# Performance work log

Measured on AMD Instinct MI355X. Metric: run time of the kernel, lower is better.

The kernel has to match this reference:

```python
import jax, jax.numpy as jnp
import numpy as np

B, T, NS, NC, M = 256, 128, 12, 4, 6
MU = 0.1                 # barrier parameter alg.mu
REG_BASE = 1.6           # fp.reg_exp_base
REG = 2.0                # bp.reg
REG_FAC = REG_BASE ** REG - 1.0


def _mt(a):
    return jnp.swapaxes(a, -1, -2)


def setup_inputs():
    key = jax.random.key(0)
    k = jax.random.split(key, 18)
    rn = lambda i, shape: jax.random.normal(k[i], shape, dtype=jnp.float32)
    eye_s = jnp.eye(NS, dtype=jnp.float32)
    eye_c = jnp.eye(NC, dtype=jnp.float32)
    fx = 0.9 * eye_s + 0.02 * rn(0, (B, T, NS, NS))
    fu = 0.1 * rn(1, (B, T, NS, NC))
    fxx = 0.01 * rn(2, (B, T, NS, NS, NS))
    fxu = 0.01 * rn(3, (B, T, NS, NS, NC))
    fuu = 0.01 * rn(4, (B, T, NS, NC, NC))
    qx = 0.1 * rn(5, (B, T, NS))
    qu = 0.1 * rn(6, (B, T, NC))
    Ax = 0.1 * rn(7, (B, T, NS, NS))
    qxx = eye_s + Ax @ _mt(Ax)            # PSD stage cost Hessian
    Au = 0.1 * rn(8, (B, T, NC, NC))
    quu = eye_c + Au @ _mt(Au)            # PD control Hessian
    qxu = 0.05 * rn(9, (B, T, NS, NC))
    cx = 0.1 * rn(10, (B, T, M, NS))
    cu = 0.1 * rn(11, (B, T, M, NC))
    # feasible iterate: c < 0 strictly, dual s > 0
    c = -(jax.random.uniform(k[12], (B, T, M), dtype=jnp.float32) + 0.1)
    s = 0.05 + 0.1 * jax.random.uniform(k[13], (B, T, M), dtype=jnp.float32)
    px = 0.1 * rn(14, (B, NS))
    P = 0.1 * rn(15, (B, NS, NS))
    pxx = eye_s + P @ _mt(P)              # PSD terminal Hessian
    return {"qx": qx, "qu": qu, "qxx": qxx, "qxu": qxu, "quu": quu,
            "fx": fx, "fu": fu, "fxx": fxx, "fxu": fxu, "fuu": fuu,
            "cx": cx, "cu": cu, "c": c, "s": s, "px": px, "pxx": pxx}


def _backward_pass(qx, qu, qxx, qxu, quu, fx, fu, fxx, fxu, fuu, cx, cu, c, s, px, pxx):
    """Feasible-branch ipddp Riccati backward recursion over T steps, batched over B."""
    Bsz = qx.shape[0]

    def step(carry, inp):
        Vx, Vxx, dV0, dV1, qu_err, mu_err = carry
        (qx_t, qu_t, qxx_t, qxu_t, quu_t, fx_t, fu_t,
         fxx_t, fxu_t, fuu_t, cx_t, cu_t, c_t, s_t) = inp
        s_col = s_t[..., None]                      # (B,M,1)
        c_col = c_t[..., None]                      # (B,M,1)
        # Q-function expansions
        Qx = qx_t[..., None] + _mt(cx_t) @ s_col + _mt(fx_t) @ Vx       # (B,NS,1)
        Qu = qu_t[..., None] + _mt(cu_t) @ s_col + _mt(fu_t) @ Vx       # (B,NC,1)
        fxV = _mt(fx_t) @ Vxx
        v = Vx[..., 0]                              # (B,NS)
        Qxx = qxx_t + fxV @ fx_t + jnp.einsum('bs,bsij->bij', v, fxx_t)
        Qxu = qxu_t + fxV @ fu_t + jnp.einsum('bs,bsij->bij', v, fxu_t)
        Quu = quu_t + _mt(fu_t) @ Vxx @ fu_t + jnp.einsum('bs,bsij->bij', v, fuu_t)
        Quu = 0.5 * (Quu + _mt(Quu))
        Quu_reg = Quu + quu_t * REG_FAC
        # interior-point (feasible) modifications
        r = s_col * c_col + MU                      # (B,M,1)
        cinv = 1.0 / c_col
        sc = (s_t / c_t)[..., None]                 # diag(SCinv) entries
        SCcu = sc * cu_t                            # SCinv @ cu
        SCcx = sc * cx_t                            # SCinv @ cx
        cuSCcu = _mt(cu_t) @ SCcu
        Qu = Qu - _mt(cu_t) @ (cinv * r)
        tempQux = _mt(Qxu) - _mt(cu_t) @ SCcx       # (B,NC,NS)
        rhs = jnp.concatenate([Qu, tempQux], axis=-1)   # (B,NC,1+NS)
        kK = -jnp.linalg.solve(Quu_reg - cuSCcu, rhs)
        ku = kK[..., :1]                            # (B,NC,1)
        Ku = kK[..., 1:]                            # (B,NC,NS)
        cuku = cu_t @ ku                            # (B,M,1)
        ks = (-cinv * (r + s_col * cuku))[..., 0]   # (B,M)
        Ks = -(sc * (cx_t + cu_t @ Ku))             # (B,M,NS)
        Quu2 = Quu - cuSCcu
        Qxu2 = _mt(tempQux)
        Qxx2 = Qxx - _mt(cx_t) @ SCcx
        Qx2 = Qx - _mt(cx_t) @ (cinv * r)
        dV0 = dV0 + (_mt(ku) @ Qu)[..., 0, 0]
        dV1 = dV1 + 0.5 * (_mt(ku) @ Quu2 @ ku)[..., 0, 0]
        QxuKu = Qxu2 @ Ku
        KtQ = _mt(Ku) @ Quu2
        Vx_new = Qx2 + _mt(Ku) @ Qu + KtQ @ ku + Qxu2 @ ku
        Vxx_new = Qxx2 + _mt(QxuKu) + QxuKu + KtQ @ Ku
        Vxx_new = 0.5 * (Vxx_new + _mt(Vxx_new))
        qu_err = jnp.maximum(qu_err, jnp.max(jnp.abs(Qu)))
        mu_err = jnp.maximum(mu_err, jnp.max(jnp.abs(r)))
        return (Vx_new, Vxx_new, dV0, dV1, qu_err, mu_err), (ku[..., 0], Ku, ks, Ks)

    xs = tuple(jnp.moveaxis(a, 1, 0) for a in
               (qx, qu, qxx, qxu, quu, fx, fu, fxx, fxu, fuu, cx, cu, c, s))
    zero = jnp.zeros((), jnp.float32)
    init = (px[..., None], pxx, jnp.zeros((Bsz,), jnp.float32),
            jnp.zeros((Bsz,), jnp.float32), zero, zero)
    carry, outs = jax.lax.scan(step, init, xs, reverse=True)
    Vx, Vxx, dV0, dV1, qu_err, mu_err = carry
    ku, Ku, ks, Ks = (jnp.moveaxis(o, 0, 1) for o in outs)
    dV = jnp.stack([dV0, dV1], axis=-1)             # (B,2)
    opterr = jnp.maximum(qu_err, mu_err)            # c_err == 0 in feasible branch
    return ku, Ku, ks, Ks, dV, opterr, Vx[..., 0], Vxx


def reference(qx, qu, qxx, qxu, quu, fx, fu, fxx, fxu, fuu, cx, cu, c, s, px, pxx):
    return _backward_pass(qx, qu, qxx, qxu, quu, fx, fu, fxx, fxu, fuu,
                          cx, cu, c, s, px, pxx)
```

## Files before the change

### kernel.cpp

```cpp
#include <hip/hip_runtime.h>
#include <cstdint>
#include <cstddef>

#define B_  256
#define T_  128
#define NS_ 12
#define NC_ 4
#define M_  6

constexpr float MU_F      = 0.1f;
constexpr float REG_FAC_F = (float)(1.6 * 1.6 - 1.0);

#define OF_FX   0
#define OF_FU   144
#define OF_FXX  192
#define OF_FXU  1920
#define OF_FUU  2496
#define OF_QXX  2688
#define OF_QXU  2832
#define OF_QUU  2880
#define OF_QX   2896
#define OF_QU   2908
#define OF_CX   2912
#define OF_CU   2984
#define OF_C    3008
#define OF_S    3014
#define STG_N   3020

#define O_KU    0
#define O_KUBIG 131072
#define O_KS    1703936
#define O_KSBIG 1900544
#define O_DV    4259840
#define O_OPT   4260352
#define O_VX    4260353
#define O_VXX   4263425

__device__ __forceinline__ void bar_lds() {
    asm volatile("s_waitcnt lgkmcnt(0)\n\ts_barrier" ::: "memory");
}

__device__ __forceinline__ void gl_lds16(const float* g, float* l) {
    __builtin_amdgcn_global_load_lds((const __attribute__((address_space(1))) void*)g,
                                     (__attribute__((address_space(3))) void*)l, 16, 0, 0);
}
__device__ __forceinline__ void gl_lds4(const float* g, float* l) {
    __builtin_amdgcn_global_load_lds((const __attribute__((address_space(1))) void*)g,
                                     (__attribute__((address_space(3))) void*)l, 4, 0, 0);
}

__global__ __launch_bounds__(256) void ddp_backward(
    const float* __restrict__ qx,  const float* __restrict__ qu,
    const float* __restrict__ qxx, const float* __restrict__ qxu,
    const float* __restrict__ quu, const float* __restrict__ fx,
    const float* __restrict__ fu,  const float* __restrict__ fxx,
    const float* __restrict__ fxu, const float* __restrict__ fuu,
    const float* __restrict__ cx,  const float* __restrict__ cu,
    const float* __restrict__ c_,  const float* __restrict__ s_,
    const float* __restrict__ px,  const float* __restrict__ pxx,
    float* __restrict__ out, float* __restrict__ ws)
{
    const int tid  = threadIdx.x;
    const int b    = blockIdx.x;
    const int lane = tid & 63;
    const int wv   = tid >> 6;

    __shared__ float stg[2][STG_N];
    __shared__ float sVx[12], sVxx[144];
    __shared__ float sfxV[144], sfuV[48];
    __shared__ float sQxx[144], sQxu[48];
    __shared__ float sQuuR[16], sQuu2[16], sM4[16];
    __shared__ float stQux[48];
    __shared__ float sQxb[12], sQub[4], sQu[4], sQx2[12];
    __shared__ float sr[6], scinv[6], ssc[6];
    __shared__ float sKu[48], sku[4], sKtQ[48];
    __shared__ float sAcc[4];

    const float* srcs[14] = {qx, qu, qxx, qxu, quu, fx, fu, fxx, fxu, fuu, cx, cu, c_, s_};

    auto prefetch = [&](float* dst, int tt) {
        const size_t bt = (size_t)b * T_ + tt;
        constexpr int ch_arr[22]  = {5,6,7,7,7,7,7,7,7,8,8,8,9,2,3,4,0,1,10,11,12,13};
        constexpr int ch_goff[22] = {0,0,0,256,512,768,1024,1280,1536,0,256,512,0,0,0,0,0,0,0,0,0,0};
        constexpr int ch_loff[22] = {OF_FX, OF_FU,
                                     OF_FXX, OF_FXX+256, OF_FXX+512, OF_FXX+768,
                                     OF_FXX+1024, OF_FXX+1280, OF_FXX+1536,
                                     OF_FXU, OF_FXU+256, OF_FXU+512,
                                     OF_FUU, OF_QXX, OF_QXU, OF_QUU, OF_QX, OF_QU,
                                     OF_CX, OF_CU, OF_C, OF_S};
        constexpr int ch_nb[22]   = {576,192,1024,1024,1024,1024,1024,1024,768,
                                     1024,1024,256,768,576,192,64,48,16,288,96,24,24};
        constexpr int sl[14]      = {12,4,144,48,16,144,48,1728,576,192,72,24,6,6};
        #pragma unroll
        for (int ci = 0; ci < 22; ++ci) {
            if ((ci & 3) == wv) {
                const float* g = srcs[ch_arr[ci]] + bt * (size_t)sl[ch_arr[ci]] + ch_goff[ci];
                float* l = dst + ch_loff[ci];
                if ((ch_nb[ci] & 15) == 0) {
                    if (lane * 16 < ch_nb[ci]) gl_lds16(g + lane * 4, l);
                } else {
                    if (lane * 4  < ch_nb[ci]) gl_lds4 (g + lane,     l);
                }
            }
        }
    };

    if (tid < 144) sVxx[tid] = pxx[(size_t)b * 144 + tid];
    if (tid < 12)  sVx[tid]  = px[(size_t)b * 12 + tid];
    if (tid == 0)  { sAcc[0] = 0.f; sAcc[1] = 0.f; sAcc[2] = 0.f; sAcc[3] = 0.f; }
    prefetch(stg[0], T_ - 1);
    __syncthreads();

    int cur = 0;
    for (int t = T_ - 1; t >= 0; --t) {
        const float* S = stg[cur];
        if (t > 0) prefetch(stg[cur ^ 1], t - 1);
        const size_t bt = (size_t)b * T_ + t;

        if (tid < 144) {
            const int i = tid / 12, k = tid % 12;
            float acc = 0.f;
            #pragma unroll
            for (int m = 0; m < 12; ++m) acc += S[OF_FX + m*12 + i] * sVxx[m*12 + k];
            sfxV[tid] = acc;
        } else if (tid < 192) {
            const int idx = tid - 144, a = idx / 12, k = idx % 12;
            float acc = 0.f;
            #pragma unroll
            for (int m = 0; m < 12; ++m) acc += S[OF_FU + m*4 + a] * sVxx[m*12 + k];
            sfuV[idx] = acc;
        } else if (tid < 198) {
            const int k = tid - 192;
            const float cc = S[OF_C + k], ssv = S[OF_S + k];
            sr[k] = ssv * cc + MU_F;
            scinv[k] = 1.0f / cc;
            ssc[k] = ssv / cc;
        } else if (tid < 210) {
            const int i = tid - 198;
            float acc = S[OF_QX + i];
            #pragma unroll
            for (int k = 0; k < 6; ++k)  acc += S[OF_CX + k*12 + i] * S[OF_S + k];
            #pragma unroll
            for (int m = 0; m < 12; ++m) acc += S[OF_FX + m*12 + i] * sVx[m];
            sQxb[i] = acc;
        } else if (tid < 214) {
            const int a = tid - 210;
            float acc = S[OF_QU + a];
            #pragma unroll
            for (int k = 0; k < 6; ++k)  acc += S[OF_CU + k*4 + a] * S[OF_S + k];
            #pragma unroll
            for (int m = 0; m < 12; ++m) acc += S[OF_FU + m*4 + a] * sVx[m];
            sQub[a] = acc;
        }
        bar_lds();

        if (tid < 144) {
            const int i = tid / 12, j = tid % 12; (void)j;
            float acc = S[OF_QXX + tid];
            #pragma unroll
            for (int k = 0; k < 12; ++k) acc += sfxV[i*12 + k] * S[OF_FX + k*12 + (tid % 12)];
            #pragma unroll
            for (int ss2 = 0; ss2 < 12; ++ss2) acc += sVx[ss2] * S[OF_FXX + ss2*144 + tid];
            sQxx[tid] = acc;
        } else if (tid < 192) {
            const int idx = tid - 144, i = idx / 4, j = idx % 4;
            float acc = S[OF_QXU + idx];
            #pragma unroll
            for (int k = 0; k < 12; ++k) acc += sfxV[i*12 + k] * S[OF_FU + k*4 + j];
            #pragma unroll
            for (int ss2 = 0; ss2 < 12; ++ss2) acc += sVx[ss2] * S[OF_FXU + ss2*48 + idx];
            sQxu[idx] = acc;
        } else if (tid < 208) {
            const int idx = tid - 192, a = idx / 4, b2 = idx % 4;
            float acc = S[OF_QUU + idx];
            #pragma unroll
            for (int k = 0; k < 12; ++k) acc += sfuV[a*12 + k] * S[OF_FU + k*4 + b2];
            #pragma unroll
            for (int ss2 = 0; ss2 < 12; ++ss2) acc += sVx[ss2] * S[OF_FUU + ss2*16 + idx];
            sQuuR[idx] = acc;
        }
        bar_lds();

        if (tid < 144) {
            const int i = tid / 12, j = tid % 12;
            float acc = sQxx[tid];
            #pragma unroll
            for (int k = 0; k < 6; ++k) acc -= S[OF_CX + k*12 + i] * ssc[k] * S[OF_CX + k*12 + j];
            sQxx[tid] = acc;
        } else if (tid < 192) {
            const int idx = tid - 144, a = idx / 12, i = idx % 12;
            float acc = sQxu[i*4 + a];
            #pragma unroll
            for (int k = 0; k < 6; ++k) acc -= S[OF_CU + k*4 + a] * ssc[k] * S[OF_CX + k*12 + i];
            stQux[idx] = acc;
        } else if (tid < 208) {
            const int idx = tid - 192, a = idx / 4, b2 = idx % 4;
            const float q = 0.5f * (sQuuR[idx] + sQuuR[b2*4 + a]);
            float cs = 0.f;
            #pragma unroll
            for (int k = 0; k < 6; ++k) cs += ssc[k] * S[OF_CU + k*4 + a] * S[OF_CU + k*4 + b2];
            const float q2 = q - cs;
            sQuu2[idx] = q2;
            sM4[idx]   = q2 + S[OF_QUU + idx] * REG_FAC_F;
        } else if (tid < 212) {
            const int a = tid - 208;
            float acc = sQub[a];
            #pragma unroll
            for (int k = 0; k < 6; ++k) acc -= S[OF_CU + k*4 + a] * scinv[k] * sr[k];
            sQu[a] = acc;
        } else if (tid < 224) {
            const int i = tid - 212;
            float acc = sQxb[i];
            #pragma unroll
            for (int k = 0; k < 6; ++k) acc -= S[OF_CX + k*12 + i] * scinv[k] * sr[k];
            sQx2[i] = acc;
        }
        bar_lds();

        if (tid < 13) {
            float a00=sM4[0],  a01=sM4[1],  a02=sM4[2],  a03=sM4[3];
            float a10=sM4[4],  a11=sM4[5],  a12=sM4[6],  a13=sM4[7];
            float a20=sM4[8],  a21=sM4[9],  a22=sM4[10], a23=sM4[11];
            float a30=sM4[12], a31=sM4[13], a32=sM4[14], a33=sM4[15];
            const float i0 = 1.0f / a00;
            const float l10 = a10*i0, l20 = a20*i0, l30 = a30*i0;
            a11 -= l10*a01; a12 -= l10*a02; a13 -= l10*a03;
            a21 -= l20*a01; a22 -= l20*a02; a23 -= l20*a03;
            a31 -= l30*a01; a32 -= l30*a02; a33 -= l30*a03;
            const float i1 = 1.0f / a11;
            const float l21 = a21*i1, l31 = a31*i1;
            a22 -= l21*a12; a23 -= l21*a13;
            a32 -= l31*a12; a33 -= l31*a13;
            const float i2 = 1.0f / a22;
            const float l32 = a32*i2;
            a33 -= l32*a23;

            float r0, r1, r2, r3;
            if (tid == 0) { r0 = sQu[0]; r1 = sQu[1]; r2 = sQu[2]; r3 = sQu[3]; }
            else { const int i = tid - 1; r0 = stQux[i]; r1 = stQux[12+i]; r2 = stQux[24+i]; r3 = stQux[36+i]; }

            const float y0 = r0;
            const float y1 = r1 - l10*y0;
            const float y2 = r2 - l20*y0 - l21*y1;
            const float y3 = r3 - l30*y0 - l31*y1 - l32*y2;
            float x3 = y3 / a33;
            float x2 = (y2 - a23*x3) * i2;
            float x1 = (y1 - a12*x2 - a13*x3) * i1;
            float x0 = (y0 - a01*x1 - a02*x2 - a03*x3) * i0;
            x0 = -x0; x1 = -x1; x2 = -x2; x3 = -x3;

            if (tid == 0) {
                sku[0]=x0; sku[1]=x1; sku[2]=x2; sku[3]=x3;
                float* kg = out + O_KU + bt*4;
                kg[0]=x0; kg[1]=x1; kg[2]=x2; kg[3]=x3;
            } else {
                const int i = tid - 1;
                sKu[i]=x0; sKu[12+i]=x1; sKu[24+i]=x2; sKu[36+i]=x3;
                float* Kg = out + O_KUBIG + bt*48;
                Kg[i]=x0; Kg[12+i]=x1; Kg[24+i]=x2; Kg[36+i]=x3;
            }
        }
        bar_lds();

        if (tid < 48) {
            const int i = tid / 4, a = tid % 4;
            float acc = 0.f;
            #pragma unroll
            for (int b2 = 0; b2 < 4; ++b2) acc += sKu[b2*12 + i] * sQuu2[b2*4 + a];
            sKtQ[tid] = acc;
        } else if (tid < 54) {
            const int k = tid - 48;
            float cuku = 0.f;
            #pragma unroll
            for (int a = 0; a < 4; ++a) cuku += S[OF_CU + k*4 + a] * sku[a];
            out[O_KS + bt*6 + k] = -scinv[k] * (sr[k] + S[OF_S + k] * cuku);
        } else if (tid < 126) {
            const int idx = tid - 54, k = idx / 12, i = idx % 12;
            float acc = S[OF_CX + k*12 + i];
            #pragma unroll
            for (int a = 0; a < 4; ++a) acc += S[OF_CU + k*4 + a] * sKu[a*12 + i];
            out[O_KSBIG + bt*72 + idx] = -(ssc[k] * acc);
        } else if (tid == 126) {
            float d = 0.f;
            #pragma unroll
            for (int a = 0; a < 4; ++a) d += sku[a] * sQu[a];
            sAcc[0] += d;
        } else if (tid == 127) {
            float d = 0.f;
            #pragma unroll
            for (int a = 0; a < 4; ++a)
                #pragma unroll
                for (int b2 = 0; b2 < 4; ++b2) d += sku[a] * sQuu2[a*4 + b2] * sku[b2];
            sAcc[1] += 0.5f * d;
        } else if (tid == 128) {
            float m = 0.f;
            #pragma unroll
            for (int a = 0; a < 4; ++a) m = fmaxf(m, fabsf(sQu[a]));
            sAcc[2] = fmaxf(sAcc[2], m);
        } else if (tid == 129) {
            float m = 0.f;
            #pragma unroll
            for (int k = 0; k < 6; ++k) m = fmaxf(m, fabsf(sr[k]));
            sAcc[3] = fmaxf(sAcc[3], m);
        }
        bar_lds();

        if (tid < 144) {
            const int i = tid / 12, j = tid % 12;
            const float v1 = sQxx[i*12 + j], v2 = sQxx[j*12 + i];
            float qk = 0.f, kk1 = 0.f, kk2 = 0.f;
            #pragma unroll
            for (int a = 0; a < 4; ++a) {
                const float kui = sKu[a*12 + i], kuj = sKu[a*12 + j];
                qk  += stQux[a*12 + i] * kuj + stQux[a*12 + j] * kui;
                kk1 += sKtQ[i*4 + a] * kuj;
                kk2 += sKtQ[j*4 + a] * kui;
            }
            sVxx[tid] = 0.5f * (v1 + v2) + qk + 0.5f * (kk1 + kk2);
        } else if (tid < 156) {
            const int i = tid - 144;
            float acc = sQx2[i];
            #pragma unroll
            for (int a = 0; a < 4; ++a)
                acc += sKu[a*12 + i] * sQu[a] + sKtQ[i*4 + a] * sku[a] + stQux[a*12 + i] * sku[a];
            sVx[i] = acc;
        }
        __syncthreads();
        cur ^= 1;
    }

    if (tid == 0) {
        out[O_DV + b*2 + 0] = sAcc[0];
        out[O_DV + b*2 + 1] = sAcc[1];
        ws[b] = fmaxf(sAcc[2], sAcc[3]);
    }
    if (tid < 12)  out[O_VX + b*12 + tid] = sVx[tid];
    if (tid < 144) out[O_VXX + (size_t)b*144 + tid] = sVxx[tid];
}

__global__ __launch_bounds__(256) void opt_reduce(const float* __restrict__ ws,
                                                  float* __restrict__ out)
{
    float v = ws[threadIdx.x];
    #pragma unroll
    for (int o = 32; o > 0; o >>= 1) v = fmaxf(v, __shfl_down(v, o, 64));
    __shared__ float m[4];
    if ((threadIdx.x & 63) == 0) m[threadIdx.x >> 6] = v;
    __syncthreads();
    if (threadIdx.x == 0) out[O_OPT] = fmaxf(fmaxf(m[0], m[1]), fmaxf(m[2], m[3]));
}

extern "C" void kernel_launch(void* const* d_in, const int* in_sizes, int n_in,
                              void* d_out, int out_size, void* d_ws, size_t ws_size,
                              hipStream_t stream) {
    const float* qx  = (const float*)d_in[0];
    const float* qu  = (const float*)d_in[1];
    const float* qxx = (const float*)d_in[2];
    const float* qxu = (const float*)d_in[3];
    const float* quu = (const float*)d_in[4];
    const float* fx  = (const float*)d_in[5];
    const float* fu  = (const float*)d_in[6];
    const float* fxx = (const float*)d_in[7];
    const float* fxu = (const float*)d_in[8];
    const float* fuu = (const float*)d_in[9];
    const float* cx  = (const float*)d_in[10];
    const float* cu  = (const float*)d_in[11];
    const float* c_  = (const float*)d_in[12];
    const float* s_  = (const float*)d_in[13];
    const float* px  = (const float*)d_in[14];
    const float* pxx = (const float*)d_in[15];
    float* out = (float*)d_out;
    float* ws  = (float*)d_ws;

    hipLaunchKernelGGL(ddp_backward, dim3(B_), dim3(256), 0, stream,
                       qx, qu, qxx, qxu, quu, fx, fu, fxx, fxu, fuu,
                       cx, cu, c_, s_, px, pxx, out, ws);
    hipLaunchKernelGGL(opt_reduce, dim3(1), dim3(256), 0, stream, ws, out);
}
```

Before: 806.0 us.

## Collapse per-batch block to a single wavefront with register-blocked float4 stages

Shrinks each batch block from four wavefronts to one 64-lane wavefront. Because all lanes are in one wave, s_barrier calls become plain lgkmcnt waits. The stages are reorganised so each lane computes four outputs with float4 LDS loads, and several phases are fused, such as the Qxx constraint correction and Qu/Qx corrections. Error and dV accumulators move into registers. The aim is to cut barrier and serial-chain latency in the T-step recursion, at the cost of fewer lanes per block and more work per lane.

```diff
diff --git a/kernel.cpp b/kernel.cpp
--- a/kernel.cpp
+++ b/kernel.cpp
@@ -36,8 +36,11 @@
 #define O_VX    4260353
 #define O_VXX   4263425
 
-__device__ __forceinline__ void bar_lds() {
-    asm volatile("s_waitcnt lgkmcnt(0)\n\ts_barrier" ::: "memory");
+__device__ __forceinline__ void wsync_lds() {
+    asm volatile("s_waitcnt lgkmcnt(0)" ::: "memory");
+}
+__device__ __forceinline__ void wsync_all() {
+    asm volatile("s_waitcnt vmcnt(0) lgkmcnt(0)" ::: "memory");
 }
 
 __device__ __forceinline__ void gl_lds16(const float* g, float* l) {
@@ -48,8 +51,10 @@
     __builtin_amdgcn_global_load_lds((const __attribute__((address_space(1))) void*)g,
                                      (__attribute__((address_space(3))) void*)l, 4, 0, 0);
 }
-
-__global__ __launch_bounds__(256) void ddp_backward(
+__device__ __forceinline__ float4 ld4(const float* p)  { return *reinterpret_cast<const float4*>(p); }
+__device__ __forceinline__ void   st4(float* p, float4 v) { *reinterpret_cast<float4*>(p) = v; }
+
+__global__ __launch_bounds__(64) void ddp_backward(
     const float* __restrict__ qx,  const float* __restrict__ qu,
     const float* __restrict__ qxx, const float* __restrict__ qxu,
     const float* __restrict__ quu, const float* __restrict__ fx,
@@ -60,26 +65,49 @@
     const float* __restrict__ px,  const float* __restrict__ pxx,
     float* __restrict__ out, float* __restrict__ ws)
 {
-    const int tid  = threadIdx.x;
-    const int b    = blockIdx.x;
-    const int lane = tid & 63;
-    const int wv   = tid >> 6;
-
-    __shared__ float stg[2][STG_N];
-    __shared__ float sVx[12], sVxx[144];
-    __shared__ float sfxV[144], sfuV[48];
-    __shared__ float sQxx[144], sQxu[48];
-    __shared__ float sQuuR[16], sQuu2[16], sM4[16];
-    __shared__ float stQux[48];
-    __shared__ float sQxb[12], sQub[4], sQu[4], sQx2[12];
-    __shared__ float sr[6], scinv[6], ssc[6];
-    __shared__ float sKu[48], sku[4], sKtQ[48];
+    const int l = threadIdx.x;
+    const int b = blockIdx.x;
+
+    __shared__ alignas(16) float stg[2][STG_N];
+    __shared__ alignas(16) float sVxx[144];
+    __shared__ alignas(16) float sVx4[48];
+    __shared__ alignas(16) float sG[192];
+    __shared__ alignas(16) float sCS[16];
+    __shared__ alignas(16) float sSC[8], sCINV[8], sR[8];
+    __shared__ alignas(16) float sOUT[192];
+    __shared__ alignas(16) float sQuuR[16], sQuu2[16], sM4[16];
+    __shared__ alignas(16) float sQP[16];
+    __shared__ alignas(16) float sku[4];
+    __shared__ alignas(16) float sKu[48];
+    __shared__ alignas(16) float sKtQ[48];
     __shared__ float sAcc[4];
 
     const float* srcs[14] = {qx, qu, qxx, qxu, quu, fx, fu, fxx, fxu, fuu, cx, cu, c_, s_};
 
+    const int up = l & 15, uq = l >> 4;
+    const int u_Fo = (up < 12) ? (OF_FX + up) : (OF_FU + up - 12);
+    const int u_Fs = (up < 12) ? 12 : 4;
+    const int p2    = l - 48;
+    const int cs_q0 = (p2 < 12) ? (OF_QX + p2) : (OF_QU + p2 - 12);
+    const int cs_cx = (p2 < 12) ? (OF_CX + p2) : (OF_CU + p2 - 12);
+    const int cs_cs = (p2 < 12) ? 12 : 4;
+    const int cs_Fo = (p2 < 12) ? (OF_FX + p2) : (OF_FU + p2 - 12);
+    const int cs_Fs = (p2 < 12) ? 12 : 4;
+    const int ai = l >> 2, apq = l & 3;
+    const bool a3 = (apq == 3);
+    const int a_q0 = a3 ? (OF_QXU + ai*4) : (OF_QXX + ai*12 + apq*4);
+    const int a_Fo = a3 ? OF_FU           : (OF_FX + apq*4);
+    const int a_Fs = a3 ? 4 : 12;
+    const int a_Xo = a3 ? (OF_FXU + ai*4) : (OF_FXX + ai*12 + apq*4);
+    const int a_Xs = a3 ? 48 : 144;
+    const int a_Co = a3 ? OF_CU           : (OF_CX + apq*4);
+    const int a_Cs = a3 ? 4 : 12;
+    const int c_cx = (l < 12) ? (OF_CX + l) : (OF_CU + l - 12);
+    const int c_cs = (l < 12) ? 12 : 4;
+    const int i5 = l / 3, jq5 = l % 3;
+
     auto prefetch = [&](float* dst, int tt) {
-        const size_t bt = (size_t)b * T_ + tt;
+        const uint32_t bt2 = (uint32_t)b * T_ + (uint32_t)tt;
         constexpr int ch_arr[22]  = {5,6,7,7,7,7,7,7,7,8,8,8,9,2,3,4,0,1,10,11,12,13};
         constexpr int ch_goff[22] = {0,0,0,256,512,768,1024,1280,1536,0,256,512,0,0,0,0,0,0,0,0,0,0};
         constexpr int ch_loff[22] = {OF_FX, OF_FU,
@@ -93,131 +121,121 @@
         constexpr int sl[14]      = {12,4,144,48,16,144,48,1728,576,192,72,24,6,6};
         #pragma unroll
         for (int ci = 0; ci < 22; ++ci) {
-            if ((ci & 3) == wv) {
-                const float* g = srcs[ch_arr[ci]] + bt * (size_t)sl[ch_arr[ci]] + ch_goff[ci];
-                float* l = dst + ch_loff[ci];
-                if ((ch_nb[ci] & 15) == 0) {
-                    if (lane * 16 < ch_nb[ci]) gl_lds16(g + lane * 4, l);
-                } else {
-                    if (lane * 4  < ch_nb[ci]) gl_lds4 (g + lane,     l);
-                }
+            const uint32_t off = bt2 * (uint32_t)sl[ch_arr[ci]] + (uint32_t)ch_goff[ci];
+            const float* g = srcs[ch_arr[ci]] + (size_t)off;
+            float* dl = dst + ch_loff[ci];
+            if ((ch_nb[ci] & 15) == 0) {
+                if (l * 16 < ch_nb[ci]) gl_lds16(g + l * 4, dl);
+            } else {
+                if (l * 4  < ch_nb[ci]) gl_lds4 (g + l,     dl);
             }
         }
     };
 
-    if (tid < 144) sVxx[tid] = pxx[(size_t)b * 144 + tid];
-    if (tid < 12)  sVx[tid]  = px[(size_t)b * 12 + tid];
-    if (tid == 0)  { sAcc[0] = 0.f; sAcc[1] = 0.f; sAcc[2] = 0.f; sAcc[3] = 0.f; }
+    for (int idx = l; idx < 144; idx += 64) sVxx[idx] = pxx[(size_t)b * 144 + idx];
+    if (l < 12) st4(sVx4 + l * 4, make_float4(px[(size_t)b * 12 + l], 0.f, 0.f, 0.f));
     prefetch(stg[0], T_ - 1);
-    __syncthreads();
-
+    wsync_all();
+
+    float dv0 = 0.f, dv1 = 0.f, qerr = 0.f, merr = 0.f;
     int cur = 0;
     for (int t = T_ - 1; t >= 0; --t) {
         const float* S = stg[cur];
         if (t > 0) prefetch(stg[cur ^ 1], t - 1);
-        const size_t bt = (size_t)b * T_ + t;
-
-        if (tid < 144) {
-            const int i = tid / 12, k = tid % 12;
-            float acc = 0.f;
-            #pragma unroll
-            for (int m = 0; m < 12; ++m) acc += S[OF_FX + m*12 + i] * sVxx[m*12 + k];
-            sfxV[tid] = acc;
-        } else if (tid < 192) {
-            const int idx = tid - 144, a = idx / 12, k = idx % 12;
-            float acc = 0.f;
-            #pragma unroll
-            for (int m = 0; m < 12; ++m) acc += S[OF_FU + m*4 + a] * sVxx[m*12 + k];
-            sfuV[idx] = acc;
-        } else if (tid < 198) {
-            const int k = tid - 192;
-            const float cc = S[OF_C + k], ssv = S[OF_S + k];
-            sr[k] = ssv * cc + MU_F;
-            scinv[k] = 1.0f / cc;
-            ssc[k] = ssv / cc;
-        } else if (tid < 210) {
-            const int i = tid - 198;
-            float acc = S[OF_QX + i];
-            #pragma unroll
-            for (int k = 0; k < 6; ++k)  acc += S[OF_CX + k*12 + i] * S[OF_S + k];
-            #pragma unroll
-            for (int m = 0; m < 12; ++m) acc += S[OF_FX + m*12 + i] * sVx[m];
-            sQxb[i] = acc;
-        } else if (tid < 214) {
-            const int a = tid - 210;
-            float acc = S[OF_QU + a];
-            #pragma unroll
-            for (int k = 0; k < 6; ++k)  acc += S[OF_CU + k*4 + a] * S[OF_S + k];
-            #pragma unroll
-            for (int m = 0; m < 12; ++m) acc += S[OF_FU + m*4 + a] * sVx[m];
-            sQub[a] = acc;
-        }
-        bar_lds();
-
-        if (tid < 144) {
-            const int i = tid / 12, j = tid % 12; (void)j;
-            float acc = S[OF_QXX + tid];
-            #pragma unroll
-            for (int k = 0; k < 12; ++k) acc += sfxV[i*12 + k] * S[OF_FX + k*12 + (tid % 12)];
-            #pragma unroll
-            for (int ss2 = 0; ss2 < 12; ++ss2) acc += sVx[ss2] * S[OF_FXX + ss2*144 + tid];
-            sQxx[tid] = acc;
-        } else if (tid < 192) {
-            const int idx = tid - 144, i = idx / 4, j = idx % 4;
-            float acc = S[OF_QXU + idx];
-            #pragma unroll
-            for (int k = 0; k < 12; ++k) acc += sfxV[i*12 + k] * S[OF_FU + k*4 + j];
-            #pragma unroll
-            for (int ss2 = 0; ss2 < 12; ++ss2) acc += sVx[ss2] * S[OF_FXU + ss2*48 + idx];
-            sQxu[idx] = acc;
-        } else if (tid < 208) {
-            const int idx = tid - 192, a = idx / 4, b2 = idx % 4;
-            float acc = S[OF_QUU + idx];
-            #pragma unroll
-            for (int k = 0; k < 12; ++k) acc += sfuV[a*12 + k] * S[OF_FU + k*4 + b2];
-            #pragma unroll
-            for (int ss2 = 0; ss2 < 12; ++ss2) acc += sVx[ss2] * S[OF_FUU + ss2*16 + idx];
-            sQuuR[idx] = acc;
-        }
-        bar_lds();
-
-        if (tid < 144) {
-            const int i = tid / 12, j = tid % 12;
-            float acc = sQxx[tid];
-            #pragma unroll
-            for (int k = 0; k < 6; ++k) acc -= S[OF_CX + k*12 + i] * ssc[k] * S[OF_CX + k*12 + j];
-            sQxx[tid] = acc;
-        } else if (tid < 192) {
-            const int idx = tid - 144, a = idx / 12, i = idx % 12;
-            float acc = sQxu[i*4 + a];
-            #pragma unroll
-            for (int k = 0; k < 6; ++k) acc -= S[OF_CU + k*4 + a] * ssc[k] * S[OF_CX + k*12 + i];
-            stQux[idx] = acc;
-        } else if (tid < 208) {
-            const int idx = tid - 192, a = idx / 4, b2 = idx % 4;
-            const float q = 0.5f * (sQuuR[idx] + sQuuR[b2*4 + a]);
-            float cs = 0.f;
-            #pragma unroll
-            for (int k = 0; k < 6; ++k) cs += ssc[k] * S[OF_CU + k*4 + a] * S[OF_CU + k*4 + b2];
-            const float q2 = q - cs;
-            sQuu2[idx] = q2;
-            sM4[idx]   = q2 + S[OF_QUU + idx] * REG_FAC_F;
-        } else if (tid < 212) {
-            const int a = tid - 208;
-            float acc = sQub[a];
-            #pragma unroll
-            for (int k = 0; k < 6; ++k) acc -= S[OF_CU + k*4 + a] * scinv[k] * sr[k];
-            sQu[a] = acc;
-        } else if (tid < 224) {
-            const int i = tid - 212;
-            float acc = sQxb[i];
-            #pragma unroll
-            for (int k = 0; k < 6; ++k) acc -= S[OF_CX + k*12 + i] * scinv[k] * sr[k];
-            sQx2[i] = acc;
-        }
-        bar_lds();
-
-        if (tid < 13) {
+        const uint32_t bt = (uint32_t)b * T_ + (uint32_t)t;
+
+        if (l < 48) {
+            const float* F   = S + u_Fo;
+            const float* col = sVxx + uq * 4;
+            float x0 = 0.f, x1 = 0.f, x2 = 0.f, x3 = 0.f;
+            #pragma unroll
+            for (int m = 0; m < 12; ++m) {
+                const float  f = F[m * u_Fs];
+                const float4 v = ld4(col + m * 12);
+                x0 += f * v.x; x1 += f * v.y; x2 += f * v.z; x3 += f * v.w;
+            }
+            st4(sG + up * 12 + uq * 4, make_float4(x0, x1, x2, x3));
+        } else {
+            float acc = S[cs_q0];
+            #pragma unroll
+            for (int k = 0; k < 6; ++k)  acc += S[cs_cx + k * cs_cs] * S[OF_S + k];
+            #pragma unroll
+            for (int m = 0; m < 12; ++m) acc += S[cs_Fo + m * cs_Fs] * sVx4[m * 4];
+            sCS[p2] = acc;
+        }
+        if (l < 6) {
+            const float cc = S[OF_C + l], sv = S[OF_S + l];
+            sR[l]    = sv * cc + MU_F;
+            sCINV[l] = 1.0f / cc;
+            sSC[l]   = sv / cc;
+        }
+        wsync_lds();
+
+        float vx[12], rsc[6], rcinv[6], rr[6];
+        #pragma unroll
+        for (int s2 = 0; s2 < 12; ++s2) vx[s2] = sVx4[s2 * 4];
+        #pragma unroll
+        for (int k = 0; k < 6; ++k) { rsc[k] = sSC[k]; rcinv[k] = sCINV[k]; rr[k] = sR[k]; }
+
+        if (l < 48) {
+            const float4 g0 = ld4(sG + ai * 12);
+            const float4 g1 = ld4(sG + ai * 12 + 4);
+            const float4 g2 = ld4(sG + ai * 12 + 8);
+            const float gk[12] = {g0.x,g0.y,g0.z,g0.w, g1.x,g1.y,g1.z,g1.w, g2.x,g2.y,g2.z,g2.w};
+            float4 acc = ld4(S + a_q0);
+            #pragma unroll
+            for (int k = 0; k < 12; ++k) {
+                const float4 f = ld4(S + a_Fo + k * a_Fs);
+                acc.x += gk[k]*f.x; acc.y += gk[k]*f.y; acc.z += gk[k]*f.z; acc.w += gk[k]*f.w;
+            }
+            #pragma unroll
+            for (int s2 = 0; s2 < 12; ++s2) {
+                const float4 xv = ld4(S + a_Xo + s2 * a_Xs);
+                acc.x += vx[s2]*xv.x; acc.y += vx[s2]*xv.y; acc.z += vx[s2]*xv.z; acc.w += vx[s2]*xv.w;
+            }
+            #pragma unroll
+            for (int k = 0; k < 6; ++k) {
+                const float t2 = rsc[k] * S[OF_CX + k * 12 + ai];
+                const float4 cv = ld4(S + a_Co + k * a_Cs);
+                acc.x -= t2*cv.x; acc.y -= t2*cv.y; acc.z -= t2*cv.z; acc.w -= t2*cv.w;
+            }
+            st4(sOUT + ai * 16 + apq * 4, acc);
+        } else if (l < 52) {
+            const int a = l - 48;
+            float4 acc = ld4(S + OF_QUU + a * 4);
+            #pragma unroll
+            for (int k = 0; k < 12; ++k) {
+                const float  g = sG[(12 + a) * 12 + k];
+                const float4 f = ld4(S + OF_FU + k * 4);
+                acc.x += g*f.x; acc.y += g*f.y; acc.z += g*f.z; acc.w += g*f.w;
+            }
+            #pragma unroll
+            for (int s2 = 0; s2 < 12; ++s2) {
+                const float4 u = ld4(S + OF_FUU + s2 * 16 + a * 4);
+                acc.x += vx[s2]*u.x; acc.y += vx[s2]*u.y; acc.z += vx[s2]*u.z; acc.w += vx[s2]*u.w;
+            }
+            st4(sQuuR + a * 4, acc);
+        }
+        if (l < 16) {
+            float acc = sCS[l];
+            #pragma unroll
+            for (int k = 0; k < 6; ++k) acc -= S[c_cx + k * c_cs] * rcinv[k] * rr[k];
+            sQP[l] = acc;
+        }
+        wsync_lds();
+        if (l >= 48) {
+            const int e = l - 48, ea = e >> 2, eb = e & 3;
+            const float q = 0.5f * (sQuuR[e] + sQuuR[eb * 4 + ea]);
+            float cs2 = 0.f;
+            #pragma unroll
+            for (int k = 0; k < 6; ++k) cs2 += rsc[k] * S[OF_CU + k*4 + ea] * S[OF_CU + k*4 + eb];
+            const float q2 = q - cs2;
+            sQuu2[e] = q2;
+            sM4[e]   = q2 + S[OF_QUU + e] * REG_FAC_F;
+        }
+        wsync_lds();
+
+        if (l < 13) {
             float a00=sM4[0],  a01=sM4[1],  a02=sM4[2],  a03=sM4[3];
             float a10=sM4[4],  a11=sM4[5],  a12=sM4[6],  a13=sM4[7];
             float a20=sM4[8],  a21=sM4[9],  a22=sM4[10], a23=sM4[11];
@@ -236,8 +254,8 @@
             a33 -= l32*a23;
 
             float r0, r1, r2, r3;
-            if (tid == 0) { r0 = sQu[0]; r1 = sQu[1]; r2 = sQu[2]; r3 = sQu[3]; }
-            else { const int i = tid - 1; r0 = stQux[i]; r1 = stQux[12+i]; r2 = stQux[24+i]; r3 = stQux[36+i]; }
+            if (l == 0) { const float4 q = ld4(sQP + 12);               r0=q.x; r1=q.y; r2=q.z; r3=q.w; }
+            else        { const float4 q = ld4(sOUT + (l-1)*16 + 12);   r0=q.x; r1=q.y; r2=q.z; r3=q.w; }
 
             const float y0 = r0;
             const float y1 = r1 - l10*y0;
@@ -249,93 +267,130 @@
             float x0 = (y0 - a01*x1 - a02*x2 - a03*x3) * i0;
             x0 = -x0; x1 = -x1; x2 = -x2; x3 = -x3;
 
-            if (tid == 0) {
+            if (l == 0) {
                 sku[0]=x0; sku[1]=x1; sku[2]=x2; sku[3]=x3;
-                float* kg = out + O_KU + bt*4;
-                kg[0]=x0; kg[1]=x1; kg[2]=x2; kg[3]=x3;
+                st4(out + O_KU + (size_t)bt * 4, make_float4(x0, x1, x2, x3));
             } else {
-                const int i = tid - 1;
+                const int i = l - 1;
                 sKu[i]=x0; sKu[12+i]=x1; sKu[24+i]=x2; sKu[36+i]=x3;
-                float* Kg = out + O_KUBIG + bt*48;
+                float* Kg = out + O_KUBIG + (size_t)bt * 48;
                 Kg[i]=x0; Kg[12+i]=x1; Kg[24+i]=x2; Kg[36+i]=x3;
             }
-        }
-        bar_lds();
-
-        if (tid < 48) {
-            const int i = tid / 4, a = tid % 4;
+        } else if (l == 56) {
+            float m = 0.f;
+            #pragma unroll
+            for (int a = 0; a < 4; ++a) m = fmaxf(m, fabsf(sQP[12 + a]));
+            qerr = fmaxf(qerr, m);
+        } else if (l == 57) {
+            float m = 0.f;
+            #pragma unroll
+            for (int k = 0; k < 6; ++k) m = fmaxf(m, fabsf(rr[k]));
+            merr = fmaxf(merr, m);
+        }
+        wsync_lds();
+
+        if (l < 48) {
             float acc = 0.f;
             #pragma unroll
-            for (int b2 = 0; b2 < 4; ++b2) acc += sKu[b2*12 + i] * sQuu2[b2*4 + a];
-            sKtQ[tid] = acc;
-        } else if (tid < 54) {
-            const int k = tid - 48;
+            for (int b2 = 0; b2 < 4; ++b2) acc += sKu[b2*12 + ai] * sQuu2[b2*4 + apq];
+            sKtQ[l] = acc;
+        }
+        if (l < 18) {
+            const int k = i5, iq = jq5;
+            const float4 cxv = ld4(S + OF_CX + k*12 + iq*4);
+            float a0 = cxv.x, a1 = cxv.y, a2 = cxv.z, a3v = cxv.w;
+            #pragma unroll
+            for (int a = 0; a < 4; ++a) {
+                const float  cua = S[OF_CU + k*4 + a];
+                const float4 kv  = ld4(sKu + a*12 + iq*4);
+                a0 += cua*kv.x; a1 += cua*kv.y; a2 += cua*kv.z; a3v += cua*kv.w;
+            }
+            const float ns = -rsc[k];
+            st4(out + O_KSBIG + (size_t)bt * 72 + k*12 + iq*4,
+                make_float4(ns*a0, ns*a1, ns*a2, ns*a3v));
+        } else if (l >= 48 && l < 54) {
+            const int k = l - 48;
             float cuku = 0.f;
             #pragma unroll
             for (int a = 0; a < 4; ++a) cuku += S[OF_CU + k*4 + a] * sku[a];
-            out[O_KS + bt*6 + k] = -scinv[k] * (sr[k] + S[OF_S + k] * cuku);
-        } else if (tid < 126) {
-            const int idx = tid - 54, k = idx / 12, i = idx % 12;
-            float acc = S[OF_CX + k*12 + i];
-            #pragma unroll
-            for (int a = 0; a < 4; ++a) acc += S[OF_CU + k*4 + a] * sKu[a*12 + i];
-            out[O_KSBIG + bt*72 + idx] = -(ssc[k] * acc);
-        } else if (tid == 126) {
+            out[O_KS + (size_t)bt * 6 + k] = -rcinv[k] * (rr[k] + S[OF_S + k] * cuku);
+        } else if (l == 54) {
             float d = 0.f;
             #pragma unroll
-            for (int a = 0; a < 4; ++a) d += sku[a] * sQu[a];
-            sAcc[0] += d;
-        } else if (tid == 127) {
+            for (int a = 0; a < 4; ++a) d += sku[a] * sQP[12 + a];
+            dv0 += d;
+        } else if (l == 55) {
             float d = 0.f;
             #pragma unroll
             for (int a = 0; a < 4; ++a)
                 #pragma unroll
                 for (int b2 = 0; b2 < 4; ++b2) d += sku[a] * sQuu2[a*4 + b2] * sku[b2];
-            sAcc[1] += 0.5f * d;
-        } else if (tid == 128) {
-            float m = 0.f;
-            #pragma unroll
-            for (int a = 0; a < 4; ++a) m = fmaxf(m, fabsf(sQu[a]));
-            sAcc[2] = fmaxf(sAcc[2], m);
-        } else if (tid == 129) {
-            float m = 0.f;
-            #pragma unroll
-            for (int k = 0; k < 6; ++k) m = fmaxf(m, fabsf(sr[k]));
-            sAcc[3] = fmaxf(sAcc[3], m);
-        }
-        bar_lds();
-
-        if (tid < 144) {
-            const int i = tid / 12, j = tid % 12;
-            const float v1 = sQxx[i*12 + j], v2 = sQxx[j*12 + i];
-            float qk = 0.f, kk1 = 0.f, kk2 = 0.f;
+            dv1 += 0.5f * d;
+        }
+        wsync_lds();
+
+        if (l < 36) {
+            const int i = i5, jq = jq5;
+            const float4 v14  = ld4(sOUT + i*16 + jq*4);
+            const float4 tqi4 = ld4(sOUT + i*16 + 12);
+            const float4 kqi4 = ld4(sKtQ + i*4);
+            const float v1[4]  = {v14.x, v14.y, v14.z, v14.w};
+            const float tqi[4] = {tqi4.x, tqi4.y, tqi4.z, tqi4.w};
+            const float kqi[4] = {kqi4.x, kqi4.y, kqi4.z, kqi4.w};
+            float kuj[4][4], kui[4];
             #pragma unroll
             for (int a = 0; a < 4; ++a) {
-                const float kui = sKu[a*12 + i], kuj = sKu[a*12 + j];
-                qk  += stQux[a*12 + i] * kuj + stQux[a*12 + j] * kui;
-                kk1 += sKtQ[i*4 + a] * kuj;
-                kk2 += sKtQ[j*4 + a] * kui;
-            }
-            sVxx[tid] = 0.5f * (v1 + v2) + qk + 0.5f * (kk1 + kk2);
-        } else if (tid < 156) {
-            const int i = tid - 144;
-            float acc = sQx2[i];
+                const float4 kv = ld4(sKu + a*12 + jq*4);
+                kuj[a][0]=kv.x; kuj[a][1]=kv.y; kuj[a][2]=kv.z; kuj[a][3]=kv.w;
+                kui[a] = sKu[a*12 + i];
+            }
+            float v2[4], tqj[4][4], kqj[4][4];
+            #pragma unroll
+            for (int r = 0; r < 4; ++r) {
+                const int j = jq*4 + r;
+                v2[r] = sOUT[j*16 + i];
+                const float4 tq = ld4(sOUT + j*16 + 12);
+                tqj[r][0]=tq.x; tqj[r][1]=tq.y; tqj[r][2]=tq.z; tqj[r][3]=tq.w;
+                const float4 kq = ld4(sKtQ + j*4);
+                kqj[r][0]=kq.x; kqj[r][1]=kq.y; kqj[r][2]=kq.z; kqj[r][3]=kq.w;
+            }
+            float res[4];
+            #pragma unroll
+            for (int r = 0; r < 4; ++r) {
+                float qk = 0.f, kk1 = 0.f, kk2 = 0.f;
+                #pragma unroll
+                for (int a = 0; a < 4; ++a) {
+                    qk  += tqi[a]*kuj[a][r] + tqj[r][a]*kui[a];
+                    kk1 += kqi[a]*kuj[a][r];
+                    kk2 += kqj[r][a]*kui[a];
+                }
+                res[r] = 0.5f*(v1[r] + v2[r]) + qk + 0.5f*(kk1 + kk2);
+            }
+            st4(sVxx + i*12 + jq*4, make_float4(res[0], res[1], res[2], res[3]));
+        } else if (l >= 48 && l < 60) {
+            const int i = l - 48;
+            float acc = sQP[i];
             #pragma unroll
             for (int a = 0; a < 4; ++a)
-                acc += sKu[a*12 + i] * sQu[a] + sKtQ[i*4 + a] * sku[a] + stQux[a*12 + i] * sku[a];
-            sVx[i] = acc;
-        }
-        __syncthreads();
+                acc += sKu[a*12+i]*sQP[12+a] + sKtQ[i*4+a]*sku[a] + sOUT[i*16+12+a]*sku[a];
+            st4(sVx4 + i*4, make_float4(acc, 0.f, 0.f, 0.f));
+        }
+        wsync_all();
         cur ^= 1;
     }
 
-    if (tid == 0) {
+    if (l == 54) sAcc[0] = dv0;
+    if (l == 55) sAcc[1] = dv1;
+    if (l == 56) sAcc[2] = qerr;
+    if (l == 57) sAcc[3] = merr;
+    wsync_lds();
+    if (l == 0) {
         out[O_DV + b*2 + 0] = sAcc[0];
         out[O_DV + b*2 + 1] = sAcc[1];
         ws[b] = fmaxf(sAcc[2], sAcc[3]);
     }
-    if (tid < 12)  out[O_VX + b*12 + tid] = sVx[tid];
-    if (tid < 144) out[O_VXX + (size_t)b*144 + tid] = sVxx[tid];
+    if (l < 12) out[O_VX + b*12 + l] = sVx4[l*4];
+    for (int idx = l; idx < 144; idx += 64) out[O_VXX + (size_t)b*144 + idx] = sVxx[idx];
 }
 
 __global__ __launch_bounds__(256) void opt_reduce(const float* __restrict__ ws,
@@ -372,7 +427,7 @@
     float* out = (float*)d_out;
     float* ws  = (float*)d_ws;
 
-    hipLaunchKernelGGL(ddp_backward, dim3(B_), dim3(256), 0, stream,
+    hipLaunchKernelGGL(ddp_backward, dim3(B_), dim3(64), 0, stream,
                        qx, qu, qxx, qxu, quu, fx, fu, fxx, fxu, fuu,
                        cx, cu, c_, s_, px, pxx, out, ws);
     hipLaunchKernelGGL(opt_reduce, dim3(1), dim3(256), 0, stream, ws, out);
```

New measurement: 829.6 us. +2.9%, slower.
